# Performance work log

Hardware: AMD Instinct MI355X
Metric: run time of the kernel (lower is better)

## Reference

```python
import jax, jax.numpy as jnp
import numpy as np

B, T, C, H, D, S = 4096, 256, 64, 16, 16, 10


def setup_inputs() -> dict:
    key = jax.random.key(0)
    ks = jax.random.split(key, 8)
    return {
        'states_seq': jax.random.uniform(ks[0], (B, T, S), dtype=jnp.float32) + 0.5,
        'covariates_seq': jax.random.normal(ks[1], (B, T, C), dtype=jnp.float32),
        'ln_gamma': jnp.ones((C,), jnp.float32),
        'ln_beta': jnp.zeros((C,), jnp.float32),
        'rnn_wx': jax.random.normal(ks[2], (C, H), dtype=jnp.float32) * 0.1,
        'rnn_wh': jax.random.normal(ks[3], (H, H), dtype=jnp.float32) * 0.1,
        'rnn_b': jnp.zeros((H,), jnp.float32),
        'd1_w': jax.random.normal(ks[4], (H, H), dtype=jnp.float32) * 0.1,
        'd1_b': jnp.zeros((H,), jnp.float32),
        'd2_w': jax.random.normal(ks[5], (H, D), dtype=jnp.float32) * 0.1,
        'd2_b': jnp.zeros((D,), jnp.float32),
    }


def _cash_budget(s, d):
    # Deterministic cash-budget accounting update.
    # s: (B, 10) = [rev_prev, cash, AR, inventory, PPE, AP, debt, equity, retained, other]
    # d: (B, 16) drivers; first 10 used as ratios.
    sig = jax.nn.sigmoid
    g      = jnp.tanh(d[:, 0]) * 0.2      # sales growth
    cogs_m = sig(d[:, 1])                 # COGS margin
    opex_m = sig(d[:, 2]) * 0.5           # opex margin
    dep_r  = sig(d[:, 3]) * 0.1           # depreciation rate on PPE
    capex_r = sig(d[:, 4]) * 0.2          # capex as % of revenue
    dso = sig(d[:, 5])                    # AR ratio
    dio = sig(d[:, 6])                    # inventory ratio
    dpo = sig(d[:, 7])                    # AP ratio
    tax_r = sig(d[:, 8]) * 0.35           # tax rate
    int_r = sig(d[:, 9]) * 0.1            # interest rate on debt

    rev_prev, cash, ar, inv, ppe, ap, debt, equity, re, other = [s[:, i] for i in range(10)]
    rev = rev_prev * (1.0 + g)
    cogs = cogs_m * rev
    opex = opex_m * rev
    dep = dep_r * ppe
    interest = int_r * debt
    ebt = rev - cogs - opex - dep - interest
    tax = tax_r * jnp.maximum(ebt, 0.0)
    ni = ebt - tax
    ar_new = dso * rev
    inv_new = dio * cogs
    ap_new = dpo * cogs
    capex = capex_r * rev
    ppe_new = ppe + capex - dep
    cash_new = cash + ni + dep - capex - (ar_new - ar) - (inv_new - inv) + (ap_new - ap)
    re_new = re + ni
    s_next = jnp.stack([rev, cash_new, ar_new, inv_new, ppe_new, ap_new, debt, equity, re_new, other], axis=-1)
    is_out = jnp.stack([rev, cogs, opex, dep, interest, tax, ni], axis=-1)  # (B, 7)
    return s_next, is_out


def reference(states_seq, covariates_seq, ln_gamma, ln_beta, rnn_wx, rnn_wh, rnn_b, d1_w, d1_b, d2_w, d2_b):
    # LayerNormalization (keras default eps=1e-3, last axis)
    mu = covariates_seq.mean(-1, keepdims=True)
    var = covariates_seq.var(-1, keepdims=True)
    x = (covariates_seq - mu) * jax.lax.rsqrt(var + 1e-3) * ln_gamma + ln_beta

    # SimpleRNN: h_t = tanh(x_t Wx + h_{t-1} Wh + b), return_sequences
    xw = jnp.einsum('btc,ch->bth', x, rnn_wx) + rnn_b  # precompute input projection

    def rnn_step(h, xt):
        h = jnp.tanh(xt + h @ rnn_wh)
        return h, h

    h0 = jnp.zeros((x.shape[0], rnn_wh.shape[0]), x.dtype)
    _, hs = jax.lax.scan(rnn_step, h0, jnp.swapaxes(xw, 0, 1))  # (T, B, H)
    hs = jnp.swapaxes(hs, 0, 1)  # (B, T, H)

    drivers = jnp.tanh(hs @ d1_w + d1_b) @ d2_w + d2_b  # (B, T, D)

    # Cash-budget recurrence over t = 1 .. T-1
    def cb_step(s_prev, d_t):
        s_next, is_out = _cash_budget(s_prev, d_t)
        return s_next, (s_next, is_out)

    s0 = states_seq[:, 0, :]
    _, (states_tm, is_tm) = jax.lax.scan(cb_step, s0, jnp.swapaxes(drivers[:, 1:, :], 0, 1))
    states_pred = jnp.swapaxes(states_tm, 0, 1)  # (B, T-1, 10)
    is_pred = jnp.swapaxes(is_tm, 0, 1)          # (B, T-1, 7)
    return states_pred, is_pred
```

## Files before the change

### kernel.cpp

```cpp
#include <hip/hip_runtime.h>
#include <hip/hip_fp16.h>

#define NB 4096
#define NT 256
#define NC 64
#define NH 16
#define NS 10
#define NTO 255

__device__ __forceinline__ float fast_rcp(float x){ return __builtin_amdgcn_rcpf(x); }
__device__ __forceinline__ float fast_rsq(float x){ return __builtin_amdgcn_rsqf(x); }
__device__ __forceinline__ float fsig(float x){ return fast_rcp(1.0f + __expf(-x)); }
__device__ __forceinline__ float ftanh(float x){
    float e = __expf(2.0f*x);
    return fmaf(-2.0f, fast_rcp(e + 1.0f), 1.0f);
}

template<int R>
__device__ __forceinline__ float rotf(float x){
    return __int_as_float(__builtin_amdgcn_update_dpp(
        0, __float_as_int(x), 0x120 + R, 0xF, 0xF, true));
}
__device__ __forceinline__ float row_bcast_sum(float x){
    x += rotf<8>(x);
    x += rotf<4>(x);
    x += rotf<2>(x);
    x += rotf<1>(x);
    return x;
}
__device__ __forceinline__ float rotdot16(float v, const float* w, float acc){
    float a1 = 0.f;
    acc = fmaf(v,          w[0],  acc);
    a1  = fmaf(rotf<1>(v), w[1],  a1);
    acc = fmaf(rotf<2>(v), w[2],  acc);
    a1  = fmaf(rotf<3>(v), w[3],  a1);
    acc = fmaf(rotf<4>(v), w[4],  acc);
    a1  = fmaf(rotf<5>(v), w[5],  a1);
    acc = fmaf(rotf<6>(v), w[6],  acc);
    a1  = fmaf(rotf<7>(v), w[7],  a1);
    acc = fmaf(rotf<8>(v), w[8],  acc);
    a1  = fmaf(rotf<9>(v), w[9],  a1);
    acc = fmaf(rotf<10>(v),w[10], acc);
    a1  = fmaf(rotf<11>(v),w[11], a1);
    acc = fmaf(rotf<12>(v),w[12], acc);
    a1  = fmaf(rotf<13>(v),w[13], a1);
    acc = fmaf(rotf<14>(v),w[14], acc);
    a1  = fmaf(rotf<15>(v),w[15], a1);
    return acc + a1;
}

__global__ __launch_bounds__(256, 4) void xw_kernel(
    const float* __restrict__ cov, const float* __restrict__ lng,
    const float* __restrict__ lnb, const float* __restrict__ wx,
    const float* __restrict__ rnb, __half* __restrict__ xws)
{
    const int wid  = threadIdx.x >> 6;
    const int lane = threadIdx.x & 63;
    const int g = lane >> 4, l = lane & 15;
    const int b = (blockIdx.x << 2) + wid;

    float gwr[64];
    #pragma unroll
    for (int r = 0; r < 16; ++r) {
        int c0 = 4 * ((l - r) & 15);
        #pragma unroll
        for (int j = 0; j < 4; ++j)
            gwr[4*r+j] = lng[c0+j] * wx[(c0+j)*NH + l];
    }
    float bwb = rnb[l];
    #pragma unroll
    for (int c = 0; c < NC; ++c) bwb = fmaf(lnb[c], wx[c*NH + l], bwb);

    const float4* gp = (const float4*)cov + (size_t)b*NT*16 + g*16 + l;
    __half* op = xws + ((size_t)b*16 + l)*NT + g;

    float4 cur = gp[0];
    float4 nxt = gp[64];
    #pragma unroll 2
    for (int it = 0; it < 64; ++it) {
        float4 x = cur;
        cur = nxt;
        if (it < 62) nxt = gp[(size_t)(it+2)*64];
        float ss = (x.x + x.y) + (x.z + x.w);
        float sq = fmaf(x.x,x.x, fmaf(x.y,x.y, fmaf(x.z,x.z, x.w*x.w)));
        ss = row_bcast_sum(ss);
        sq = row_bcast_sum(sq);
        float mu  = ss * (1.0f/64.0f);
        float var = fmaf(-mu, mu, sq * (1.0f/64.0f));
        float rs  = fast_rsq(var + 0.001f);
        float nmu = -mu * rs;
        float x0 = fmaf(x.x, rs, nmu), x1 = fmaf(x.y, rs, nmu);
        float x2 = fmaf(x.z, rs, nmu), x3 = fmaf(x.w, rs, nmu);
        float a0 = bwb, a1 = 0.f, a2 = 0.f, a3 = 0.f;
        a0 = fmaf(x0, gwr[0], a0); a1 = fmaf(x1, gwr[1], a1);
        a2 = fmaf(x2, gwr[2], a2); a3 = fmaf(x3, gwr[3], a3);
#define ROTSTEP(R) { float r0=rotf<R>(x0), r1=rotf<R>(x1), r2=rotf<R>(x2), r3=rotf<R>(x3); \
        a0=fmaf(r0,gwr[4*R+0],a0); a1=fmaf(r1,gwr[4*R+1],a1); \
        a2=fmaf(r2,gwr[4*R+2],a2); a3=fmaf(r3,gwr[4*R+3],a3); }
        ROTSTEP(1)  ROTSTEP(2)  ROTSTEP(3)  ROTSTEP(4)  ROTSTEP(5)
        ROTSTEP(6)  ROTSTEP(7)  ROTSTEP(8)  ROTSTEP(9)  ROTSTEP(10)
        ROTSTEP(11) ROTSTEP(12) ROTSTEP(13) ROTSTEP(14) ROTSTEP(15)
#undef ROTSTEP
        float xw = (a0+a1)+(a2+a3);
        op[it*4] = __float2half(xw);
    }
}

__global__ __launch_bounds__(64, 1) void scan_kernel(
    const float* __restrict__ states, const __half* __restrict__ xws,
    const float* __restrict__ wh,     const float* __restrict__ d1w,
    const float* __restrict__ d1b,    const float* __restrict__ d2w,
    const float* __restrict__ d2b,    float* __restrict__ out)
{
    const int lane = threadIdx.x;
    const int g = lane >> 4, l = lane & 15;
    const int b = (blockIdx.x << 2) + g;

    __shared__ __align__(16) float db[64];

    float whr[NH], d1r[NH], d2r[NH];
    #pragma unroll
    for (int r = 0; r < NH; ++r) {
        int src = (l - r) & 15;
        whr[r] = wh[src*NH + l];
        d1r[r] = d1w[src*NH + l];
        d2r[r] = d2w[src*NH + l];
    }
    const float d1bl = d1b[l], d2bl = d2b[l];
    const float Aa = (l==0)?0.4f:(l==2)?0.5f:(l==3)?0.1f:(l==4)?0.2f:(l==8)?0.35f:(l==9)?0.1f:1.0f;
    const float Ba = (l==0)?2.0f:1.0f;
    const float Ca = (l==0)?-0.2f:0.0f;

    float s0,s1,s2,s3,s4,s5,s6,s7,s8,s9;
    { const float* sp = states + (size_t)b*NT*NS;
      s0=sp[0];s1=sp[1];s2=sp[2];s3=sp[3];s4=sp[4];
      s5=sp[5];s6=sp[6];s7=sp[7];s8=sp[8];s9=sp[9]; }

    float* spo = out + (size_t)b*NTO*NS + l;
    float* ipo = out + (size_t)NB*NTO*NS + (size_t)b*NTO*7 + l;

    const ushort4* xp = (const ushort4*)(xws + ((size_t)b*16 + l)*NT);
    ushort4 xa = xp[0], xb = xp[1];

    float h = 0.f;
    #pragma unroll 1
    for (int tt = 0; tt < 64; ++tt) {
        ushort4 xc = xa; xa = xb;
        if (tt < 62) xb = xp[tt+2];
        #pragma unroll
        for (int u = 0; u < 4; ++u) {
            const int t = tt*4 + u;
            float xwv = __half2float(__ushort_as_half(u==0?xc.x:u==1?xc.y:u==2?xc.z:xc.w));
            h = ftanh(rotdot16(h, whr, xwv));
            if (t > 0) {
                float t1  = ftanh(rotdot16(h, d1r, d1bl));
                float dv  = rotdot16(t1, d2r, d2bl);
                float act = fmaf(Aa, fsig(Ba * dv), Ca);
                db[lane] = act;
                float4 w0 = *((const float4*)db + g*4);
                float4 w1 = *((const float4*)db + g*4 + 1);
                float2 w2 = *((const float2*)(db + g*16 + 8));

                float rev   = fmaf(s0, w0.x, s0);
                float cogs  = w0.y * rev;
                float opex  = w0.z * rev;
                float dep   = w0.w * s4;
                float inte  = w2.y * s6;
                float ebt   = (((rev - cogs) - opex) - dep) - inte;
                float tax   = w2.x * fmaxf(ebt, 0.0f);
                float ni    = ebt - tax;
                float arn   = w1.y * rev;
                float invn  = w1.z * cogs;
                float apn   = w1.w * cogs;
                float capex = w1.x * rev;
                float ppen  = (s4 + capex) - dep;
                float cashn = (((((s1 + ni) + dep) - capex) - (arn - s2)) - (invn - s3)) + (apn - s5);
                float ren   = s8 + ni;

                s0=rev; s1=cashn; s2=arn; s3=invn; s4=ppen; s5=apn; s8=ren;

                float sv = (l==0)?rev:(l==1)?cashn:(l==2)?arn:(l==3)?invn:(l==4)?ppen:
                           (l==5)?apn:(l==6)?s6:(l==7)?s7:(l==8)?ren:s9;
                float iv = (l==0)?rev:(l==1)?cogs:(l==2)?opex:(l==3)?dep:(l==4)?inte:(l==5)?tax:ni;
                if (l < NS) *spo = sv;
                if (l < 7)  *ipo = iv;
                spo += NS; ipo += 7;
            }
        }
    }
}

extern "C" void kernel_launch(void* const* d_in, const int* in_sizes, int n_in,
                              void* d_out, int out_size, void* d_ws, size_t ws_size,
                              hipStream_t stream) {
    (void)in_sizes; (void)n_in; (void)ws_size; (void)out_size;
    __half* xws = (__half*)d_ws;
    xw_kernel<<<NB/4, 256, 0, stream>>>(
        (const float*)d_in[1],
        (const float*)d_in[2],
        (const float*)d_in[3],
        (const float*)d_in[4],
        (const float*)d_in[6],
        xws);
    scan_kernel<<<NB/4, 64, 0, stream>>>(
        (const float*)d_in[0],
        xws,
        (const float*)d_in[5],
        (const float*)d_in[7],
        (const float*)d_in[8],
        (const float*)d_in[9],
        (const float*)d_in[10],
        (float*)d_out);
}
```

Before: 600.7 us.

## Software-pipeline RNN recurrence with dense head and cash budget across time chunks

After: 595.7 us. Within noise of the previous version (-0.8%).

```diff
diff --git a/kernel.cpp b/kernel.cpp
--- a/kernel.cpp
+++ b/kernel.cpp
@@ -7,6 +7,8 @@
 #define NH 16
 #define NS 10
 #define NTO 255
+#define TC 8
+#define NCHUNK (NT/TC)
 
 __device__ __forceinline__ float fast_rcp(float x){ return __builtin_amdgcn_rcpf(x); }
 __device__ __forceinline__ float fast_rsq(float x){ return __builtin_amdgcn_rsqf(x); }
@@ -47,6 +49,13 @@
     acc = fmaf(rotf<14>(v),w[14], acc);
     a1  = fmaf(rotf<15>(v),w[15], a1);
     return acc + a1;
+}
+
+__device__ __forceinline__ float xw_at(float4 v, int u){
+    unsigned w = (u<2) ? __float_as_uint(v.x) : (u<4) ? __float_as_uint(v.y)
+               : (u<6) ? __float_as_uint(v.z) : __float_as_uint(v.w);
+    unsigned hh = (u & 1) ? (w >> 16) : (w & 0xffffu);
+    return __half2float(__ushort_as_half((unsigned short)hh));
 }
 
 __global__ __launch_bounds__(256, 4) void xw_kernel(
@@ -116,7 +125,7 @@
     const int g = lane >> 4, l = lane & 15;
     const int b = (blockIdx.x << 2) + g;
 
-    __shared__ __align__(16) float db[64];
+    __shared__ __align__(16) float db[2*TC*64];
 
     float whr[NH], d1r[NH], d2r[NH];
     #pragma unroll
@@ -139,55 +148,91 @@
     float* spo = out + (size_t)b*NTO*NS + l;
     float* ipo = out + (size_t)NB*NTO*NS + (size_t)b*NTO*7 + l;
 
-    const ushort4* xp = (const ushort4*)(xws + ((size_t)b*16 + l)*NT);
-    ushort4 xa = xp[0], xb = xp[1];
+    const float4* xp = (const float4*)(xws + ((size_t)b*16 + l)*NT);
+    float4 xcur = xp[0];
+    float4 xnxt = xp[1];
 
     float h = 0.f;
+    float hA[TC], hB[TC];
+
+#define PH1(DST) \
+    _Pragma("unroll") \
+    for (int u = 0; u < TC; ++u) { h = ftanh(rotdot16(h, whr, xw_at(xcur,u))); DST[u] = h; }
+
+#define PH2(DBK) \
+    _Pragma("unroll") \
+    for (int u = 0; u < TC; ++u) { \
+        float t1  = ftanh(rotdot16(hA[u], d1r, d1bl)); \
+        float dv  = rotdot16(t1, d2r, d2bl); \
+        (DBK)[u*64 + lane] = fmaf(Aa, fsig(Ba*dv), Ca); \
+    }
+
+#define BUDGET(DBK, U) do { \
+    float4 w0 = *((const float4*)((DBK) + (U)*64 + g*16)); \
+    float4 w1 = *((const float4*)((DBK) + (U)*64 + g*16 + 4)); \
+    float2 w2 = *((const float2*)((DBK) + (U)*64 + g*16 + 8)); \
+    float rev   = fmaf(s0, w0.x, s0); \
+    float cogs  = w0.y * rev; \
+    float opex  = w0.z * rev; \
+    float dep   = w0.w * s4; \
+    float inte  = w2.y * s6; \
+    float ebt   = (((rev - cogs) - opex) - dep) - inte; \
+    float tax   = w2.x * fmaxf(ebt, 0.0f); \
+    float ni    = ebt - tax; \
+    float arn   = w1.y * rev; \
+    float invn  = w1.z * cogs; \
+    float apn   = w1.w * cogs; \
+    float capex = w1.x * rev; \
+    float ppen  = (s4 + capex) - dep; \
+    float cashn = (((((s1 + ni) + dep) - capex) - (arn - s2)) - (invn - s3)) + (apn - s5); \
+    float ren   = s8 + ni; \
+    s0=rev; s1=cashn; s2=arn; s3=invn; s4=ppen; s5=apn; s8=ren; \
+    float sv = (l==0)?rev:(l==1)?cashn:(l==2)?arn:(l==3)?invn:(l==4)?ppen: \
+               (l==5)?apn:(l==6)?s6:(l==7)?s7:(l==8)?ren:s9; \
+    float iv = (l==0)?rev:(l==1)?cogs:(l==2)?opex:(l==3)?dep:(l==4)?inte:(l==5)?tax:ni; \
+    if (l < NS) *spo = sv; \
+    if (l < 7)  *ipo = iv; \
+    spo += NS; ipo += 7; \
+} while(0)
+
+    PH1(hA)
+    xcur = xnxt;
+    xnxt = xp[2];
+
+    {
+        PH1(hB)
+        float* dbk = db;
+        PH2(dbk)
+        #pragma unroll
+        for (int u = 1; u < TC; ++u) BUDGET(dbk, u);
+        #pragma unroll
+        for (int u = 0; u < TC; ++u) hA[u] = hB[u];
+        xcur = xnxt;
+    }
+
     #pragma unroll 1
-    for (int tt = 0; tt < 64; ++tt) {
-        ushort4 xc = xa; xa = xb;
-        if (tt < 62) xb = xp[tt+2];
-        #pragma unroll
-        for (int u = 0; u < 4; ++u) {
-            const int t = tt*4 + u;
-            float xwv = __half2float(__ushort_as_half(u==0?xc.x:u==1?xc.y:u==2?xc.z:xc.w));
-            h = ftanh(rotdot16(h, whr, xwv));
-            if (t > 0) {
-                float t1  = ftanh(rotdot16(h, d1r, d1bl));
-                float dv  = rotdot16(t1, d2r, d2bl);
-                float act = fmaf(Aa, fsig(Ba * dv), Ca);
-                db[lane] = act;
-                float4 w0 = *((const float4*)db + g*4);
-                float4 w1 = *((const float4*)db + g*4 + 1);
-                float2 w2 = *((const float2*)(db + g*16 + 8));
-
-                float rev   = fmaf(s0, w0.x, s0);
-                float cogs  = w0.y * rev;
-                float opex  = w0.z * rev;
-                float dep   = w0.w * s4;
-                float inte  = w2.y * s6;
-                float ebt   = (((rev - cogs) - opex) - dep) - inte;
-                float tax   = w2.x * fmaxf(ebt, 0.0f);
-                float ni    = ebt - tax;
-                float arn   = w1.y * rev;
-                float invn  = w1.z * cogs;
-                float apn   = w1.w * cogs;
-                float capex = w1.x * rev;
-                float ppen  = (s4 + capex) - dep;
-                float cashn = (((((s1 + ni) + dep) - capex) - (arn - s2)) - (invn - s3)) + (apn - s5);
-                float ren   = s8 + ni;
-
-                s0=rev; s1=cashn; s2=arn; s3=invn; s4=ppen; s5=apn; s8=ren;
-
-                float sv = (l==0)?rev:(l==1)?cashn:(l==2)?arn:(l==3)?invn:(l==4)?ppen:
-                           (l==5)?apn:(l==6)?s6:(l==7)?s7:(l==8)?ren:s9;
-                float iv = (l==0)?rev:(l==1)?cogs:(l==2)?opex:(l==3)?dep:(l==4)?inte:(l==5)?tax:ni;
-                if (l < NS) *spo = sv;
-                if (l < 7)  *ipo = iv;
-                spo += NS; ipo += 7;
-            }
-        }
-    }
+    for (int k = 1; k < NCHUNK-1; ++k) {
+        xnxt = xp[(k+2 < NCHUNK) ? (k+2) : (NCHUNK-1)];
+        PH1(hB)
+        float* dbk = db + (k & 1)*(TC*64);
+        PH2(dbk)
+        #pragma unroll
+        for (int u = 0; u < TC; ++u) BUDGET(dbk, u);
+        #pragma unroll
+        for (int u = 0; u < TC; ++u) hA[u] = hB[u];
+        xcur = xnxt;
+    }
+
+    {
+        float* dbk = db + ((NCHUNK-1) & 1)*(TC*64);
+        PH2(dbk)
+        #pragma unroll
+        for (int u = 0; u < TC; ++u) BUDGET(dbk, u);
+    }
+
+#undef PH1
+#undef PH2
+#undef BUDGET
 }
 
 extern "C" void kernel_launch(void* const* d_in, const int* in_sizes, int n_in,
```

## Split fused scan into separate RNN, parallel MLP and budget recurrence kernels

Applied to the files above, without the earlier changes.

Result: slower. 621.2 us (+3.4%).

```diff
diff --git a/kernel.cpp b/kernel.cpp
--- a/kernel.cpp
+++ b/kernel.cpp
@@ -7,6 +7,11 @@
 #define NH 16
 #define NS 10
 #define NTO 255
+
+#define XWS_BYTES  33554432ull
+#define H_BYTES    67108864ull
+#define ACT_BYTES  41943040ull
+#define WS_NEEDED  (XWS_BYTES + H_BYTES + ACT_BYTES)
 
 __device__ __forceinline__ float fast_rcp(float x){ return __builtin_amdgcn_rcpf(x); }
 __device__ __forceinline__ float fast_rsq(float x){ return __builtin_amdgcn_rsqf(x); }
@@ -47,6 +52,17 @@
     acc = fmaf(rotf<14>(v),w[14], acc);
     a1  = fmaf(rotf<15>(v),w[15], a1);
     return acc + a1;
+}
+
+__device__ __forceinline__ float xw_at(float4 v, int u){
+    unsigned w = (u<2) ? __float_as_uint(v.x) : (u<4) ? __float_as_uint(v.y)
+               : (u<6) ? __float_as_uint(v.z) : __float_as_uint(v.w);
+    unsigned hh = (u & 1) ? (w >> 16) : (w & 0xffffu);
+    return __half2float(__ushort_as_half((unsigned short)hh));
+}
+
+__device__ __forceinline__ float comp4(float4 v, int c){
+    return c==0 ? v.x : c==1 ? v.y : c==2 ? v.z : v.w;
 }
 
 __global__ __launch_bounds__(256, 4) void xw_kernel(
@@ -106,7 +122,146 @@
     }
 }
 
-__global__ __launch_bounds__(64, 1) void scan_kernel(
+__global__ __launch_bounds__(64, 1) void rnn_kernel(
+    const __half* __restrict__ xws, const float* __restrict__ wh,
+    float* __restrict__ hbuf)
+{
+    const int lane = threadIdx.x;
+    const int g = lane >> 4, l = lane & 15;
+    const int b = (blockIdx.x << 2) + g;
+
+    float whr[NH];
+    #pragma unroll
+    for (int r = 0; r < NH; ++r) whr[r] = wh[((l - r) & 15)*NH + l];
+
+    const float4* xp = (const float4*)(xws + ((size_t)b*16 + l)*NT);
+    float* hp = hbuf + (size_t)b*NT*16 + l;
+
+    float4 xa = xp[0], xb = xp[1];
+    float h = 0.f;
+    #pragma unroll 1
+    for (int tt = 0; tt < 32; ++tt) {
+        float4 xc = xa; xa = xb;
+        if (tt < 30) xb = xp[tt+2];
+        float* hst = hp + (size_t)tt*128;
+        #pragma unroll
+        for (int u = 0; u < 8; ++u) {
+            h = ftanh(rotdot16(h, whr, xw_at(xc, u)));
+            hst[u*16] = h;
+        }
+    }
+}
+
+__global__ __launch_bounds__(256, 4) void mlp_kernel(
+    const float* __restrict__ hbuf, const float* __restrict__ d1w,
+    const float* __restrict__ d1b,  const float* __restrict__ d2w,
+    const float* __restrict__ d2b,  float* __restrict__ act)
+{
+    const int wid  = threadIdx.x >> 6;
+    const int lane = threadIdx.x & 63;
+    const int g = lane >> 4, l = lane & 15;
+    const int b = (blockIdx.x << 2) + wid;
+
+    float d1r[NH], d2r[NH];
+    #pragma unroll
+    for (int r = 0; r < NH; ++r) {
+        int src = (l - r) & 15;
+        d1r[r] = d1w[src*NH + l];
+        d2r[r] = d2w[src*NH + l];
+    }
+    const float d1bl = d1b[l], d2bl = d2b[l];
+    const float Aa = (l==0)?0.4f:(l==2)?0.5f:(l==3)?0.1f:(l==4)?0.2f:(l==8)?0.35f:(l==9)?0.1f:1.0f;
+    const float Ba = (l==0)?2.0f:1.0f;
+    const float Ca = (l==0)?-0.2f:0.0f;
+
+    const float* hp = hbuf + ((size_t)b*NT + g)*16 + l;
+    float* ap = act + ((size_t)b*NT + g)*10 + l;
+
+    float hcur = hp[0];
+    float hnxt = hp[64];
+    #pragma unroll 4
+    for (int k = 0; k < 64; ++k) {
+        float hv = hcur; hcur = hnxt;
+        if (k < 62) hnxt = hp[(k+2)*64];
+        float t1 = ftanh(rotdot16(hv, d1r, d1bl));
+        float dv = rotdot16(t1, d2r, d2bl);
+        float av = fmaf(Aa, fsig(Ba*dv), Ca);
+        if (l < NS) ap[k*40] = av;
+    }
+}
+
+__global__ __launch_bounds__(64, 1) void budget_kernel(
+    const float* __restrict__ states, const float* __restrict__ act,
+    float* __restrict__ out)
+{
+    const int lane = threadIdx.x;
+    const int g = lane >> 4, l = lane & 15;
+    const int b = (blockIdx.x << 2) + g;
+
+    float s0,s1,s2,s3,s4,s5,s6,s7,s8,s9;
+    { const float* sp = states + (size_t)b*NT*NS;
+      s0=sp[0];s1=sp[1];s2=sp[2];s3=sp[3];s4=sp[4];
+      s5=sp[5];s6=sp[6];s7=sp[7];s8=sp[8];s9=sp[9]; }
+
+    float* spo = out + (size_t)b*NTO*NS + l;
+    float* ipo = out + (size_t)NB*NTO*NS + (size_t)b*NTO*7 + l;
+
+    const float4* gp4 = (const float4*)(act + (size_t)b*NT*10);
+
+    float4 ca[10], cb[10];
+
+#define DD(BUF,J,I) comp4(BUF[((J)*10+(I))>>2], ((J)*10+(I))&3)
+
+#define BSTEP(BUF,J) do { \
+    float d0=DD(BUF,J,0), d1=DD(BUF,J,1), d2=DD(BUF,J,2), d3=DD(BUF,J,3), d4=DD(BUF,J,4); \
+    float d5=DD(BUF,J,5), d6=DD(BUF,J,6), d7=DD(BUF,J,7), d8=DD(BUF,J,8), d9=DD(BUF,J,9); \
+    float rev   = fmaf(s0, d0, s0); \
+    float cogs  = d1 * rev; \
+    float opex  = d2 * rev; \
+    float dep   = d3 * s4; \
+    float inte  = d9 * s6; \
+    float ebt   = (((rev - cogs) - opex) - dep) - inte; \
+    float tax   = d8 * fmaxf(ebt, 0.0f); \
+    float ni    = ebt - tax; \
+    float arn   = d5 * rev; \
+    float invn  = d6 * cogs; \
+    float apn   = d7 * cogs; \
+    float capex = d4 * rev; \
+    float ppen  = (s4 + capex) - dep; \
+    float cashn = (((((s1 + ni) + dep) - capex) - (arn - s2)) - (invn - s3)) + (apn - s5); \
+    float ren   = s8 + ni; \
+    s0=rev; s1=cashn; s2=arn; s3=invn; s4=ppen; s5=apn; s8=ren; \
+    float sv = (l==0)?rev:(l==1)?cashn:(l==2)?arn:(l==3)?invn:(l==4)?ppen: \
+               (l==5)?apn:(l==6)?s6:(l==7)?s7:(l==8)?ren:s9; \
+    float iv = (l==0)?rev:(l==1)?cogs:(l==2)?opex:(l==3)?dep:(l==4)?inte:(l==5)?tax:ni; \
+    if (l < NS) *spo = sv; \
+    if (l < 7)  *ipo = iv; \
+    spo += NS; ipo += 7; \
+} while(0)
+
+#define LOADG(BUF, K) { _Pragma("unroll") \
+    for (int q = 0; q < 10; ++q) BUF[q] = gp4[(size_t)(K)*10 + q]; }
+
+    LOADG(ca, 0)
+    LOADG(cb, 1)
+    BSTEP(ca,1); BSTEP(ca,2); BSTEP(ca,3);
+    LOADG(ca, 2)
+
+    #pragma unroll 1
+    for (int k = 1; k <= 61; k += 2) {
+        BSTEP(cb,0); BSTEP(cb,1); BSTEP(cb,2); BSTEP(cb,3);
+        LOADG(cb, k+2)
+        BSTEP(ca,0); BSTEP(ca,1); BSTEP(ca,2); BSTEP(ca,3);
+        if (k+3 < 64) LOADG(ca, k+3)
+    }
+    BSTEP(cb,0); BSTEP(cb,1); BSTEP(cb,2); BSTEP(cb,3);
+
+#undef LOADG
+#undef BSTEP
+#undef DD
+}
+
+__global__ __launch_bounds__(64, 1) void scan_fallback(
     const float* __restrict__ states, const __half* __restrict__ xws,
     const float* __restrict__ wh,     const float* __restrict__ d1w,
     const float* __restrict__ d1b,    const float* __restrict__ d2w,
@@ -193,7 +348,7 @@
 extern "C" void kernel_launch(void* const* d_in, const int* in_sizes, int n_in,
                               void* d_out, int out_size, void* d_ws, size_t ws_size,
                               hipStream_t stream) {
-    (void)in_sizes; (void)n_in; (void)ws_size; (void)out_size;
+    (void)in_sizes; (void)n_in; (void)out_size;
     __half* xws = (__half*)d_ws;
     xw_kernel<<<NB/4, 256, 0, stream>>>(
         (const float*)d_in[1],
@@ -202,13 +357,29 @@
         (const float*)d_in[4],
         (const float*)d_in[6],
         xws);
-    scan_kernel<<<NB/4, 64, 0, stream>>>(
-        (const float*)d_in[0],
-        xws,
-        (const float*)d_in[5],
-        (const float*)d_in[7],
-        (const float*)d_in[8],
-        (const float*)d_in[9],
-        (const float*)d_in[10],
-        (float*)d_out);
-}
+    if (ws_size >= WS_NEEDED) {
+        float* hbuf = (float*)((char*)d_ws + XWS_BYTES);
+        float* actb = (float*)((char*)d_ws + XWS_BYTES + H_BYTES);
+        rnn_kernel<<<NB/4, 64, 0, stream>>>(
+            xws, (const float*)d_in[5], hbuf);
+        mlp_kernel<<<NB/4, 256, 0, stream>>>(
+            hbuf,
+            (const float*)d_in[7],
+            (const float*)d_in[8],
+            (const float*)d_in[9],
+            (const float*)d_in[10],
+            actb);
+        budget_kernel<<<NB/4, 64, 0, stream>>>(
+            (const float*)d_in[0], actb, (float*)d_out);
+    } else {
+        scan_fallback<<<NB/4, 64, 0, stream>>>(
+            (const float*)d_in[0],
+            xws,
+            (const float*)d_in[5],
+            (const float*)d_in[7],
+            (const float*)d_in[8],
+            (const float*)d_in[9],
+            (const float*)d_in[10],
+            (float*)d_out);
+    }
+}
```

## Software-pipeline RNN, MLP and cash-budget stages across timesteps in scan kernel

Applied to the files above, without the earlier changes.

After: 589.0 us. About the same (-1.9%).

```diff
diff --git a/kernel.cpp b/kernel.cpp
--- a/kernel.cpp
+++ b/kernel.cpp
@@ -28,25 +28,25 @@
     x += rotf<1>(x);
     return x;
 }
-__device__ __forceinline__ float rotdot16(float v, const float* w, float acc){
-    float a1 = 0.f;
-    acc = fmaf(v,          w[0],  acc);
-    a1  = fmaf(rotf<1>(v), w[1],  a1);
-    acc = fmaf(rotf<2>(v), w[2],  acc);
-    a1  = fmaf(rotf<3>(v), w[3],  a1);
-    acc = fmaf(rotf<4>(v), w[4],  acc);
-    a1  = fmaf(rotf<5>(v), w[5],  a1);
-    acc = fmaf(rotf<6>(v), w[6],  acc);
-    a1  = fmaf(rotf<7>(v), w[7],  a1);
-    acc = fmaf(rotf<8>(v), w[8],  acc);
-    a1  = fmaf(rotf<9>(v), w[9],  a1);
-    acc = fmaf(rotf<10>(v),w[10], acc);
-    a1  = fmaf(rotf<11>(v),w[11], a1);
-    acc = fmaf(rotf<12>(v),w[12], acc);
-    a1  = fmaf(rotf<13>(v),w[13], a1);
-    acc = fmaf(rotf<14>(v),w[14], acc);
-    a1  = fmaf(rotf<15>(v),w[15], a1);
-    return acc + a1;
+__device__ __forceinline__ float rotdot16_4(float v, const float* w, float acc){
+    float a1 = 0.f, a2 = 0.f, a3 = 0.f;
+    acc = fmaf(v,           w[0],  acc);
+    a1  = fmaf(rotf<1>(v),  w[1],  a1);
+    a2  = fmaf(rotf<2>(v),  w[2],  a2);
+    a3  = fmaf(rotf<3>(v),  w[3],  a3);
+    acc = fmaf(rotf<4>(v),  w[4],  acc);
+    a1  = fmaf(rotf<5>(v),  w[5],  a1);
+    a2  = fmaf(rotf<6>(v),  w[6],  a2);
+    a3  = fmaf(rotf<7>(v),  w[7],  a3);
+    acc = fmaf(rotf<8>(v),  w[8],  acc);
+    a1  = fmaf(rotf<9>(v),  w[9],  a1);
+    a2  = fmaf(rotf<10>(v), w[10], a2);
+    a3  = fmaf(rotf<11>(v), w[11], a3);
+    acc = fmaf(rotf<12>(v), w[12], acc);
+    a1  = fmaf(rotf<13>(v), w[13], a1);
+    a2  = fmaf(rotf<14>(v), w[14], a2);
+    a3  = fmaf(rotf<15>(v), w[15], a3);
+    return (acc + a1) + (a2 + a3);
 }
 
 __global__ __launch_bounds__(256, 4) void xw_kernel(
@@ -116,7 +116,7 @@
     const int g = lane >> 4, l = lane & 15;
     const int b = (blockIdx.x << 2) + g;
 
-    __shared__ __align__(16) float db[64];
+    __shared__ __align__(16) float db[8*64];
 
     float whr[NH], d1r[NH], d2r[NH];
     #pragma unroll
@@ -143,51 +143,76 @@
     ushort4 xa = xp[0], xb = xp[1];
 
     float h = 0.f;
+
+#define BSLOT(T) (((T)&7)<<6)
+
+#define RNN(XWV)  h = ftanh(rotdot16_4(h, whr, (XWV)))
+
+#define MLP(T) do { \
+    float t1 = ftanh(rotdot16_4(h, d1r, d1bl)); \
+    float dv = rotdot16_4(t1, d2r, d2bl); \
+    db[BSLOT(T) + lane] = fmaf(Aa, fsig(Ba*dv), Ca); \
+} while(0)
+
+#define BUDGET(T) do { \
+    const float* rb = db + BSLOT(T) + (g<<4); \
+    float4 w0 = *(const float4*)rb; \
+    float4 w1 = *(const float4*)(rb+4); \
+    float2 w2 = *(const float2*)(rb+8); \
+    float rev   = fmaf(s0, w0.x, s0); \
+    float cogs  = w0.y * rev; \
+    float opex  = w0.z * rev; \
+    float dep   = w0.w * s4; \
+    float inte  = w2.y * s6; \
+    float ebt   = (((rev - cogs) - opex) - dep) - inte; \
+    float tax   = w2.x * fmaxf(ebt, 0.0f); \
+    float ni    = ebt - tax; \
+    float arn   = w1.y * rev; \
+    float invn  = w1.z * cogs; \
+    float apn   = w1.w * cogs; \
+    float capex = w1.x * rev; \
+    float ppen  = (s4 + capex) - dep; \
+    float cashn = (((((s1 + ni) + dep) - capex) - (arn - s2)) - (invn - s3)) + (apn - s5); \
+    float ren   = s8 + ni; \
+    s0=rev; s1=cashn; s2=arn; s3=invn; s4=ppen; s5=apn; s8=ren; \
+    float sv = (l==0)?rev:(l==1)?cashn:(l==2)?arn:(l==3)?invn:(l==4)?ppen: \
+               (l==5)?apn:(l==6)?s6:(l==7)?s7:(l==8)?ren:s9; \
+    float iv = (l==0)?rev:(l==1)?cogs:(l==2)?opex:(l==3)?dep:(l==4)?inte:(l==5)?tax:ni; \
+    if (l < NS) *spo = sv; \
+    if (l < 7)  *ipo = iv; \
+    spo += NS; ipo += 7; \
+} while(0)
+
+#define XH(V,U) __half2float(__ushort_as_half((U)==0?(V).x:(U)==1?(V).y:(U)==2?(V).z:(V).w))
+
+    {
+        ushort4 xc = xa; xa = xb; xb = xp[2];
+        RNN(XH(xc,0));
+        RNN(XH(xc,1)); MLP(1);
+        RNN(XH(xc,2)); BUDGET(1); MLP(2);
+        RNN(XH(xc,3)); BUDGET(2); MLP(3);
+    }
+
     #pragma unroll 1
-    for (int tt = 0; tt < 64; ++tt) {
+    for (int tt = 1; tt < 64; ++tt) {
         ushort4 xc = xa; xa = xb;
         if (tt < 62) xb = xp[tt+2];
         #pragma unroll
         for (int u = 0; u < 4; ++u) {
             const int t = tt*4 + u;
-            float xwv = __half2float(__ushort_as_half(u==0?xc.x:u==1?xc.y:u==2?xc.z:xc.w));
-            h = ftanh(rotdot16(h, whr, xwv));
-            if (t > 0) {
-                float t1  = ftanh(rotdot16(h, d1r, d1bl));
-                float dv  = rotdot16(t1, d2r, d2bl);
-                float act = fmaf(Aa, fsig(Ba * dv), Ca);
-                db[lane] = act;
-                float4 w0 = *((const float4*)db + g*4);
-                float4 w1 = *((const float4*)db + g*4 + 1);
-                float2 w2 = *((const float2*)(db + g*16 + 8));
-
-                float rev   = fmaf(s0, w0.x, s0);
-                float cogs  = w0.y * rev;
-                float opex  = w0.z * rev;
-                float dep   = w0.w * s4;
-                float inte  = w2.y * s6;
-                float ebt   = (((rev - cogs) - opex) - dep) - inte;
-                float tax   = w2.x * fmaxf(ebt, 0.0f);
-                float ni    = ebt - tax;
-                float arn   = w1.y * rev;
-                float invn  = w1.z * cogs;
-                float apn   = w1.w * cogs;
-                float capex = w1.x * rev;
-                float ppen  = (s4 + capex) - dep;
-                float cashn = (((((s1 + ni) + dep) - capex) - (arn - s2)) - (invn - s3)) + (apn - s5);
-                float ren   = s8 + ni;
-
-                s0=rev; s1=cashn; s2=arn; s3=invn; s4=ppen; s5=apn; s8=ren;
-
-                float sv = (l==0)?rev:(l==1)?cashn:(l==2)?arn:(l==3)?invn:(l==4)?ppen:
-                           (l==5)?apn:(l==6)?s6:(l==7)?s7:(l==8)?ren:s9;
-                float iv = (l==0)?rev:(l==1)?cogs:(l==2)?opex:(l==3)?dep:(l==4)?inte:(l==5)?tax:ni;
-                if (l < NS) *spo = sv;
-                if (l < 7)  *ipo = iv;
-                spo += NS; ipo += 7;
-            }
+            RNN(XH(xc,u));
+            BUDGET(t-1);
+            MLP(t);
         }
     }
+
+    BUDGET(255);
+
+#undef XH
+#undef BUDGET
+#undef MLP
+#undef RNN
+#undef BSLOT
 }
 
 extern "C" void kernel_launch(void* const* d_in, const int* in_sizes, int n_in,
```
